# Performance work log

Hardware: AMD Instinct MI355X
Metric: run time of the kernel (lower is better)

## Reference

```python
import jax, jax.numpy as jnp
import numpy as np

T, S, B, E, H, F = 100, 4096, 32, 256, 8, 2048
DH = E // H
EPS = 1e-5

def setup_inputs() -> dict:
    key = jax.random.key(0)
    ks = jax.random.split(key, 32)
    n = lambda i, shape, s=1.0: jax.random.normal(ks[i], shape, jnp.float32) * s
    inp = {
        'hidden_states': n(0, (T, B, E)),
        'query_pos': n(1, (T, B, E)),
        'enc_hidden': n(2, (S, B, E)),
        'enc_pos': n(3, (S, B, E)),
        'attn_mask': n(4, (B * H, T, S)),
        # cross-attn (nn.MultiheadAttention) params
        'ca_wq': n(5, (E, E), 0.02), 'ca_bq': jnp.zeros(E),
        'ca_wk': n(6, (E, E), 0.02), 'ca_bk': jnp.zeros(E),
        'ca_wv': n(7, (E, E), 0.02), 'ca_bv': jnp.zeros(E),
        'ca_wo': n(8, (E, E), 0.02), 'ca_bo': jnp.zeros(E),
        # self-attn (Mask2FormerAttention) params
        'sa_wq': n(9, (E, E), 0.02), 'sa_bq': jnp.zeros(E),
        'sa_wk': n(10, (E, E), 0.02), 'sa_bk': jnp.zeros(E),
        'sa_wv': n(11, (E, E), 0.02), 'sa_bv': jnp.zeros(E),
        'sa_wo': n(12, (E, E), 0.02), 'sa_bo': jnp.zeros(E),
        # layer norms
        'ln1_g': jnp.ones(E), 'ln1_b': jnp.zeros(E),
        'ln2_g': jnp.ones(E), 'ln2_b': jnp.zeros(E),
        'ln3_g': jnp.ones(E), 'ln3_b': jnp.zeros(E),
        # FFN
        'fc1_w': n(13, (F, E), 0.02), 'fc1_b': jnp.zeros(F),
        'fc2_w': n(14, (E, F), 0.02), 'fc2_b': jnp.zeros(E),
    }
    return inp

def _ln(x, g, b):
    m = jnp.mean(x, -1, keepdims=True)
    v = jnp.mean(jnp.square(x - m), -1, keepdims=True)
    return (x - m) * jax.lax.rsqrt(v + EPS) * g + b

def _mha(q_in, k_in, v_in, wq, bq, wk, bk, wv, bv, wo, bo, mask):
    # q_in: [B,T,E], k_in/v_in: [B,S,E], mask: [B*H,T,S] additive or None
    b, t, _ = q_in.shape
    s = k_in.shape[1]
    q = (q_in @ wq.T + bq) * (DH ** -0.5)
    k = k_in @ wk.T + bk
    v = v_in @ wv.T + bv
    q = q.reshape(b, t, H, DH).transpose(0, 2, 1, 3)  # [B,H,T,dh]
    k = k.reshape(b, s, H, DH).transpose(0, 2, 1, 3)
    v = v.reshape(b, s, H, DH).transpose(0, 2, 1, 3)
    scores = jnp.einsum('bhtd,bhsd->bhts', q, k)
    if mask is not None:
        scores = scores + mask.reshape(b, H, t, s)
    p = jax.nn.softmax(scores, axis=-1)
    o = jnp.einsum('bhts,bhsd->bhtd', p, v)
    o = o.transpose(0, 2, 1, 3).reshape(b, t, E)
    return o @ wo.T + bo

def reference(hidden_states, query_pos, enc_hidden, enc_pos, attn_mask,
              ca_wq, ca_bq, ca_wk, ca_bk, ca_wv, ca_bv, ca_wo, ca_bo,
              sa_wq, sa_bq, sa_wk, sa_bk, sa_wv, sa_bv, sa_wo, sa_bo,
              ln1_g, ln1_b, ln2_g, ln2_b, ln3_g, ln3_b,
              fc1_w, fc1_b, fc2_w, fc2_b):
    # convert seq-first [T,B,E] -> batch-first [B,T,E]
    hs = hidden_states.transpose(1, 0, 2)
    qp = query_pos.transpose(1, 0, 2)
    enc = enc_hidden.transpose(1, 0, 2)
    ep = enc_pos.transpose(1, 0, 2)
    # masked cross-attention (post-norm), dropout=0
    residual = hs
    x = _mha(hs + qp, enc + ep, enc,
             ca_wq, ca_bq, ca_wk, ca_bk, ca_wv, ca_bv, ca_wo, ca_bo, attn_mask)
    hs = _ln(residual + x, ln1_g, ln1_b)
    # self-attention with query pos embeddings on q and k, no mask
    residual = hs
    x = _mha(hs + qp, hs + qp, hs,
             sa_wq, sa_bq, sa_wk, sa_bk, sa_wv, sa_bv, sa_wo, sa_bo, None)
    hs = _ln(residual + x, ln2_g, ln2_b)
    # FFN
    x = jax.nn.relu(hs @ fc1_w.T + fc1_b) @ fc2_w.T + fc2_b
    hs = _ln(hs + x, ln3_g, ln3_b)
    return hs.transpose(1, 0, 2)  # back to [T,B,E]
```

## Files before the change

### kernel.cpp

```cpp
#include <hip/hip_runtime.h>
#include <hip/hip_bf16.h>
#include <math.h>

#define TQ 100
#define SS 4096
#define BB 32
#define EE 256
#define HH 8
#define FF 2048
#define DHH 32
#define LNEPS 1e-5f

typedef __attribute__((ext_vector_type(8))) short bf16x8;
typedef __attribute__((ext_vector_type(4))) short bf16x4;
typedef __attribute__((ext_vector_type(4))) float f32x4;

__device__ inline unsigned short f2bfu(float f) {
    __hip_bfloat16 h = __float2bfloat16(f);
    return *reinterpret_cast<unsigned short*>(&h);
}

#define PBM 64
#define PBK 32
#define PLDP 40
#define TLP 268

__global__ __launch_bounds__(256)
void cvt_all(const float* s0, const float* s1, const float* s2, const float* s3,
             const float* s4, const float* s5, const float* s6, const float* s7,
             const float* s8, const float* s9,
             unsigned short* d0, unsigned short* d1, unsigned short* d2, unsigned short* d3,
             unsigned short* d4, unsigned short* d5, unsigned short* d6, unsigned short* d7,
             unsigned short* d8, unsigned short* d9)
{
    const int bi = blockIdx.x;
    const float* s; unsigned short* d; int base;
    if (bi < 512) {
        const int seg = bi >> 6;
        base = (bi & 63) * 1024;
        switch (seg) {
            case 0: s = s0; d = d0; break;
            case 1: s = s1; d = d1; break;
            case 2: s = s2; d = d2; break;
            case 3: s = s3; d = d3; break;
            case 4: s = s4; d = d4; break;
            case 5: s = s5; d = d5; break;
            case 6: s = s6; d = d6; break;
            default: s = s7; d = d7; break;
        }
    } else {
        const int r = bi - 512;
        base = (r & 511) * 1024;
        if (r >> 9) { s = s9; d = d9; } else { s = s8; d = d8; }
    }
    const int i = base + threadIdx.x * 4;
    float4 v = *(const float4*)(s + i);
    ushort4 ov;
    ov.x = f2bfu(v.x); ov.y = f2bfu(v.y); ov.z = f2bfu(v.z); ov.w = f2bfu(v.w);
    *(ushort4*)(d + i) = ov;
}

__global__ __launch_bounds__(512, 4)
void proj_kv(const float* __restrict__ enc, const float* __restrict__ ep,
             const __hip_bfloat16* __restrict__ Wk, const float* __restrict__ bk,
             const __hip_bfloat16* __restrict__ Wv, const float* __restrict__ bv,
             __hip_bfloat16* __restrict__ Kout, __hip_bfloat16* __restrict__ Vtout)
{
    __shared__ short Akv[PBM][PLDP];
    __shared__ short Av[PBM][PLDP];
    __shared__ short BkRaw[256 * PLDP];
    __shared__ short BvRaw[256 * PLDP];
    short (*Bk)[PLDP] = (short(*)[PLDP])BkRaw;
    short (*Bv)[PLDP] = (short(*)[PLDP])BvRaw;
    short (*tk)[TLP] = (short(*)[TLP])BkRaw;
    short (*tv)[TLP] = (short(*)[TLP])BvRaw;

    const int tid = threadIdx.x;
    const int m0 = blockIdx.x * PBM;
    const int b = m0 >> 12;
    const int s0 = m0 & (SS - 1);

    const int arr = tid >> 3;
    const int arc = (tid & 7) << 2;
    const long long abase = ((long long)(s0 + arr) * BB + b) * EE + arc;
    const int wr = tid >> 1;
    const int wc = (tid & 1) << 4;
    const long long wbase = (long long)wr * EE + wc;

    const int w = tid >> 6, l = tid & 63;
    const int mat = w >> 2;
    const int wm0 = (w & 1) * 32;
    const int wn0 = ((w >> 1) & 1) * 128;
    const int lr16 = l & 15, lk8 = (l >> 4) * 8;

    f32x4 acc[2][8] = {};

    float4 a0 = *(const float4*)(enc + abase);
    float4 e0 = *(const float4*)(ep + abase);

    for (int k0 = 0; k0 < EE; k0 += PBK) {
        bf16x8 wk8a = *(const bf16x8*)(Wk + wbase + k0);
        bf16x8 wk8b = *(const bf16x8*)(Wk + wbase + k0 + 8);
        bf16x8 wv8a = *(const bf16x8*)(Wv + wbase + k0);
        bf16x8 wv8b = *(const bf16x8*)(Wv + wbase + k0 + 8);

        bf16x4 pv, pkv;
        pv[0] = (short)f2bfu(a0.x); pv[1] = (short)f2bfu(a0.y);
        pv[2] = (short)f2bfu(a0.z); pv[3] = (short)f2bfu(a0.w);
        pkv[0] = (short)f2bfu(a0.x + e0.x); pkv[1] = (short)f2bfu(a0.y + e0.y);
        pkv[2] = (short)f2bfu(a0.z + e0.z); pkv[3] = (short)f2bfu(a0.w + e0.w);

        __syncthreads();
        *(bf16x4*)&Akv[arr][arc] = pkv;
        *(bf16x4*)&Av[arr][arc]  = pv;
        *(bf16x8*)&Bk[wr][wc]     = wk8a;
        *(bf16x8*)&Bk[wr][wc + 8] = wk8b;
        *(bf16x8*)&Bv[wr][wc]     = wv8a;
        *(bf16x8*)&Bv[wr][wc + 8] = wv8b;
        __syncthreads();

        if (k0 + PBK < EE) {
            a0 = *(const float4*)(enc + abase + k0 + PBK);
            e0 = *(const float4*)(ep + abase + k0 + PBK);
        }

        const short (*Am)[PLDP] = mat ? Av : Akv;
        const short (*Bm)[PLDP] = mat ? Bv : Bk;
        bf16x8 af0 = *(const bf16x8*)&Am[wm0 + lr16][lk8];
        bf16x8 af1 = *(const bf16x8*)&Am[wm0 + 16 + lr16][lk8];
        #pragma unroll
        for (int j = 0; j < 8; ++j) {
            bf16x8 b8 = *(const bf16x8*)&Bm[wn0 + j * 16 + lr16][lk8];
            acc[0][j] = __builtin_amdgcn_mfma_f32_16x16x32_bf16(af0, b8, acc[0][j], 0, 0, 0);
            acc[1][j] = __builtin_amdgcn_mfma_f32_16x16x32_bf16(af1, b8, acc[1][j], 0, 0, 0);
        }
    }

    const float* bias = mat ? bv : bk;
    const int q4 = (l >> 4) * 4;
    #pragma unroll
    for (int h = 0; h < 2; ++h) {
        __syncthreads();
        if (wm0 == h * 32) {
            short (*tile)[TLP] = mat ? tv : tk;
            #pragma unroll
            for (int i = 0; i < 2; ++i) {
                #pragma unroll
                for (int j = 0; j < 8; ++j) {
                    const int n = wn0 + j * 16 + lr16;
                    const float bi = bias[n];
                    #pragma unroll
                    for (int r = 0; r < 4; ++r)
                        tile[i * 16 + q4 + r][n] = (short)f2bfu(acc[i][j][r] + bi);
                }
            }
        }
        __syncthreads();
        #pragma unroll
        for (int it = 0; it < 4; ++it) {
            const int r2 = w * 4 + it;
            ushort4 v = *(const ushort4*)&tk[r2][l * 4];
            *(ushort4*)(Kout + (long long)(m0 + h * 32 + r2) * EE + l * 4) = v;
        }
        #pragma unroll
        for (int nn = 0; nn < 16; ++nn) {
            const int n = w * 32 + nn * 2 + (l >> 5);
            const int s = l & 31;
            unsigned short v = (unsigned short)tv[s][n];
            *((unsigned short*)Vtout + (long long)(b * EE + n) * SS + s0 + h * 32 + s) = v;
        }
    }
}

template<int A1G, int A2Q, int A1BF, int OBF, int RELU>
__global__ __launch_bounds__(128)
void mfma_gemm2(const void* __restrict__ A1v, const float* __restrict__ A2,
                const __hip_bfloat16* __restrict__ Wb, const float* __restrict__ bias,
                void* __restrict__ outv, int N, int K, float scale)
{
    __shared__ short As[32][PLDP];
    __shared__ short Bs[128][PLDP];
    const int tid = threadIdx.x;
    const int m0 = blockIdx.x * 32;
    const int n0 = blockIdx.y * 128;
    const int rr = tid >> 2;
    const int rc = (tid & 3) << 3;
    const int row = m0 + rr;

    long long a2row = 0;
    if (A1G || A2Q) {
        int bq = row / TQ, tq = row - bq * TQ;
        a2row = ((long long)(tq * BB + bq)) * EE;
    }
    const long long a1row = A1G ? a2row : (long long)row * K;

    const int wv = tid >> 6, l = tid & 63;
    const int wm0 = wv * 16;
    const int lr16 = l & 15, lk8 = (l >> 4) * 8;

    f32x4 acc[8] = {};

    for (int k0 = 0; k0 < K; k0 += PBK) {
        bf16x8 apack;
        if (A1BF) {
            apack = *(const bf16x8*)((const __hip_bfloat16*)A1v + a1row + k0 + rc);
        } else {
            const float* A1 = (const float*)A1v;
            float4 a0 = *(const float4*)(A1 + a1row + k0 + rc);
            float4 a1 = *(const float4*)(A1 + a1row + k0 + rc + 4);
            if (A2Q) {
                float4 e0 = *(const float4*)(A2 + a2row + k0 + rc);
                float4 e1 = *(const float4*)(A2 + a2row + k0 + rc + 4);
                a0.x += e0.x; a0.y += e0.y; a0.z += e0.z; a0.w += e0.w;
                a1.x += e1.x; a1.y += e1.y; a1.z += e1.z; a1.w += e1.w;
            }
            apack[0] = (short)f2bfu(a0.x); apack[1] = (short)f2bfu(a0.y);
            apack[2] = (short)f2bfu(a0.z); apack[3] = (short)f2bfu(a0.w);
            apack[4] = (short)f2bfu(a1.x); apack[5] = (short)f2bfu(a1.y);
            apack[6] = (short)f2bfu(a1.z); apack[7] = (short)f2bfu(a1.w);
        }

        bf16x8 wreg[4];
        #pragma unroll
        for (int it = 0; it < 4; ++it)
            wreg[it] = *(const bf16x8*)(Wb + (long long)(n0 + rr + it * 32) * K + k0 + rc);

        __syncthreads();
        *(bf16x8*)&As[rr][rc] = apack;
        #pragma unroll
        for (int it = 0; it < 4; ++it)
            *(bf16x8*)&Bs[rr + it * 32][rc] = wreg[it];
        __syncthreads();

        bf16x8 af = *(const bf16x8*)&As[wm0 + lr16][lk8];
        #pragma unroll
        for (int j = 0; j < 8; ++j) {
            bf16x8 bfr = *(const bf16x8*)&Bs[j * 16 + lr16][lk8];
            acc[j] = __builtin_amdgcn_mfma_f32_16x16x32_bf16(af, bfr, acc[j], 0, 0, 0);
        }
    }

    const int q4 = (l >> 4) * 4;
    #pragma unroll
    for (int j = 0; j < 8; ++j) {
        const int n = n0 + j * 16 + lr16;
        const float bi = bias[n];
        #pragma unroll
        for (int r = 0; r < 4; ++r) {
            float v = (acc[j][r] + bi) * scale;
            if (RELU) v = fmaxf(v, 0.f);
            const long long oidx = (long long)(m0 + wm0 + q4 + r) * N + n;
            if (OBF) ((__hip_bfloat16*)outv)[oidx] = __float2bfloat16(v);
            else     ((float*)outv)[oidx] = v;
        }
    }
}

__global__ __launch_bounds__(128)
void qkv_sa(const float* __restrict__ hs1, const float* __restrict__ qp,
            const __hip_bfloat16* __restrict__ Wq, const float* __restrict__ bq,
            const __hip_bfloat16* __restrict__ Wk, const float* __restrict__ bk,
            const __hip_bfloat16* __restrict__ Wv, const float* __restrict__ bv,
            __hip_bfloat16* __restrict__ Qs, __hip_bfloat16* __restrict__ Ks,
            __hip_bfloat16* __restrict__ Vt, int SVT, float qscale)
{
    __shared__ short Aq[32][PLDP];
    __shared__ short Av[32][PLDP];
    __shared__ short Bq[128][PLDP];
    __shared__ short Bk[128][PLDP];
    __shared__ short Bv[128][PLDP];
    const int tid = threadIdx.x;
    const int m0 = blockIdx.x * 32;
    const int n0 = blockIdx.y * 128;
    const int rr = tid >> 2;
    const int rc = (tid & 3) << 3;
    const int row = m0 + rr;
    const int bq_ = row / TQ, tq = row - bq_ * TQ;
    const long long a1row = (long long)row * EE;
    const long long a2row = ((long long)(tq * BB + bq_)) * EE;

    const int wv = tid >> 6, l = tid & 63;
    const int wm0 = wv * 16;
    const int lr16 = l & 15, lk8 = (l >> 4) * 8;

    f32x4 aq[8] = {}, ak[8] = {}, av[8] = {};

    for (int k0 = 0; k0 < EE; k0 += PBK) {
        float4 a0 = *(const float4*)(hs1 + a1row + k0 + rc);
        float4 a1 = *(const float4*)(hs1 + a1row + k0 + rc + 4);
        float4 e0 = *(const float4*)(qp + a2row + k0 + rc);
        float4 e1 = *(const float4*)(qp + a2row + k0 + rc + 4);
        bf16x8 pq, pv;
        pv[0] = (short)f2bfu(a0.x); pv[1] = (short)f2bfu(a0.y);
        pv[2] = (short)f2bfu(a0.z); pv[3] = (short)f2bfu(a0.w);
        pv[4] = (short)f2bfu(a1.x); pv[5] = (short)f2bfu(a1.y);
        pv[6] = (short)f2bfu(a1.z); pv[7] = (short)f2bfu(a1.w);
        pq[0] = (short)f2bfu(a0.x + e0.x); pq[1] = (short)f2bfu(a0.y + e0.y);
        pq[2] = (short)f2bfu(a0.z + e0.z); pq[3] = (short)f2bfu(a0.w + e0.w);
        pq[4] = (short)f2bfu(a1.x + e1.x); pq[5] = (short)f2bfu(a1.y + e1.y);
        pq[6] = (short)f2bfu(a1.z + e1.z); pq[7] = (short)f2bfu(a1.w + e1.w);

        bf16x8 wq8[4], wk8[4], wv8[4];
        #pragma unroll
        for (int it = 0; it < 4; ++it) {
            const long long wr = (long long)(n0 + rr + it * 32) * EE + k0 + rc;
            wq8[it] = *(const bf16x8*)(Wq + wr);
            wk8[it] = *(const bf16x8*)(Wk + wr);
            wv8[it] = *(const bf16x8*)(Wv + wr);
        }

        __syncthreads();
        *(bf16x8*)&Aq[rr][rc] = pq;
        *(bf16x8*)&Av[rr][rc] = pv;
        #pragma unroll
        for (int it = 0; it < 4; ++it) {
            *(bf16x8*)&Bq[rr + it * 32][rc] = wq8[it];
            *(bf16x8*)&Bk[rr + it * 32][rc] = wk8[it];
            *(bf16x8*)&Bv[rr + it * 32][rc] = wv8[it];
        }
        __syncthreads();

        bf16x8 afq = *(const bf16x8*)&Aq[wm0 + lr16][lk8];
        bf16x8 afv = *(const bf16x8*)&Av[wm0 + lr16][lk8];
        #pragma unroll
        for (int j = 0; j < 8; ++j) {
            bf16x8 b1 = *(const bf16x8*)&Bq[j * 16 + lr16][lk8];
            bf16x8 b2 = *(const bf16x8*)&Bk[j * 16 + lr16][lk8];
            bf16x8 b3 = *(const bf16x8*)&Bv[j * 16 + lr16][lk8];
            aq[j] = __builtin_amdgcn_mfma_f32_16x16x32_bf16(afq, b1, aq[j], 0, 0, 0);
            ak[j] = __builtin_amdgcn_mfma_f32_16x16x32_bf16(afq, b2, ak[j], 0, 0, 0);
            av[j] = __builtin_amdgcn_mfma_f32_16x16x32_bf16(afv, b3, av[j], 0, 0, 0);
        }
    }

    const int q4 = (l >> 4) * 4;
    #pragma unroll
    for (int j = 0; j < 8; ++j) {
        const int n = n0 + j * 16 + lr16;
        const float b1 = bq[n], b2 = bk[n], b3 = bv[n];
        #pragma unroll
        for (int r = 0; r < 4; ++r) {
            const int m = m0 + wm0 + q4 + r;
            Qs[(long long)m * EE + n] = __float2bfloat16((aq[j][r] + b1) * qscale);
            Ks[(long long)m * EE + n] = __float2bfloat16(ak[j][r] + b2);
            const int bb = m / TQ, tt = m - bb * TQ;
            Vt[(long long)(bb * EE + n) * SVT + tt] = __float2bfloat16(av[j][r] + b3);
        }
    }
}

#define KVB 32
#define LDP 40

__global__ __launch_bounds__(256, 2)
void flash_mfma(const __hip_bfloat16* __restrict__ Qg,
                const __hip_bfloat16* __restrict__ Kg,
                const __hip_bfloat16* __restrict__ Vtg,
                const float* __restrict__ mask,
                __hip_bfloat16* __restrict__ O,
                int Skv, int SVT)
{
    __shared__ short Ks[2][KVB][LDP];
    __shared__ short Vs[2][KVB][LDP];
    const int tid = threadIdx.x;
    const int l = tid & 63;
    const int g = l >> 4, q16 = l & 15;
    const int chunk = gridDim.x >> 3;
    const int logical = (blockIdx.x & 7) * chunk + (blockIdx.x >> 3);
    const int qb = logical & 1;
    const int bh = logical >> 1;
    const int h = bh & (HH - 1), b = bh >> 3;
    const int q0 = qb * 64 + (tid >> 6) * 16;

    int qc = q0 + q16; if (qc >= TQ) qc = TQ - 1;
    const bf16x8 qfrag = *(const bf16x8*)(Qg + ((long long)(b * TQ + qc)) * EE + h * DHH + g * 8);

    const int srow = tid >> 3;
    const int sseg = (tid & 7) * 4;
    const long long kbase = ((long long)b * Skv) * EE + h * DHH;
    const long long vbase = ((long long)(b * EE + h * DHH)) * SVT;
    const float* mrowp = mask ? mask + ((long long)bh * TQ + qc) * Skv : nullptr;

    f32x4 oacc[2] = {{0.f,0.f,0.f,0.f},{0.f,0.f,0.f,0.f}};
    float mrun = -1e30f, lrun = 0.f;
    const f32x4 zero = {0.f,0.f,0.f,0.f};

    int s_ld = srow; if (s_ld >= Skv) s_ld = Skv - 1;
    bf16x4 kreg = *(const bf16x4*)(Kg + kbase + (long long)s_ld * EE + sseg);
    bf16x4 vreg = *(const bf16x4*)(Vtg + vbase + (long long)srow * SVT + sseg);
    float4 mcur0, mcur1;
    if (mrowp) {
        mcur0 = *(const float4*)(mrowp + g * 4);
        mcur1 = *(const float4*)(mrowp + 16 + g * 4);
    }

    const int nround = (Skv + KVB - 1) / KVB;
    for (int r = 0; r < nround; ++r) {
        const int buf = r & 1;
        *(bf16x4*)&Ks[buf][srow][sseg] = kreg;
        *(bf16x4*)&Vs[buf][srow][sseg] = vreg;
        float4 mnx0, mnx1;
        if (r + 1 < nround) {
            int sn = (r + 1) * KVB + srow; if (sn >= Skv) sn = Skv - 1;
            kreg = *(const bf16x4*)(Kg + kbase + (long long)sn * EE + sseg);
            vreg = *(const bf16x4*)(Vtg + vbase + (long long)srow * SVT + (r + 1) * KVB + sseg);
            if (mrowp) {
                mnx0 = *(const float4*)(mrowp + (r + 1) * KVB + g * 4);
                mnx1 = *(const float4*)(mrowp + (r + 1) * KVB + 16 + g * 4);
            }
        }
        __syncthreads();

        const int s0 = r * KVB;
        f32x4 sT[2];
        #pragma unroll
        for (int t = 0; t < 2; ++t) {
            bf16x8 kf = *(const bf16x8*)&Ks[buf][t * 16 + q16][g * 8];
            sT[t] = __builtin_amdgcn_mfma_f32_16x16x32_bf16(kf, qfrag, zero, 0, 0, 0);
        }
        float sc[8];
        if (mrowp) {
            sc[0] = sT[0][0] + mcur0.x; sc[1] = sT[0][1] + mcur0.y;
            sc[2] = sT[0][2] + mcur0.z; sc[3] = sT[0][3] + mcur0.w;
            sc[4] = sT[1][0] + mcur1.x; sc[5] = sT[1][1] + mcur1.y;
            sc[6] = sT[1][2] + mcur1.z; sc[7] = sT[1][3] + mcur1.w;
        } else {
            #pragma unroll
            for (int t = 0; t < 2; ++t)
                #pragma unroll
                for (int rg = 0; rg < 4; ++rg) {
                    int s = s0 + t * 16 + g * 4 + rg;
                    sc[t*4+rg] = (s < Skv) ? sT[t][rg] : -1e30f;
                }
        }
        float tmax = sc[0];
        #pragma unroll
        for (int i = 1; i < 8; ++i) tmax = fmaxf(tmax, sc[i]);
        tmax = fmaxf(tmax, __shfl_xor(tmax, 16));
        tmax = fmaxf(tmax, __shfl_xor(tmax, 32));
        const float mn = fmaxf(mrun, tmax);
        const float corr = __expf(mrun - mn);
        mrun = mn;
        float ps = 0.f;
        bf16x8 pfrag;
        #pragma unroll
        for (int i = 0; i < 8; ++i) {
            float p = __expf(sc[i] - mn);
            ps += p;
            pfrag[i] = (short)f2bfu(p);
        }
        ps += __shfl_xor(ps, 16);
        ps += __shfl_xor(ps, 32);
        lrun = lrun * corr + ps;
        #pragma unroll
        for (int rg = 0; rg < 4; ++rg) {
            float c = __shfl(corr, g * 4 + rg);
            oacc[0][rg] *= c;
            oacc[1][rg] *= c;
        }
        #pragma unroll
        for (int T = 0; T < 2; ++T) {
            bf16x4 v0 = *(const bf16x4*)&Vs[buf][T * 16 + q16][g * 4];
            bf16x4 v1 = *(const bf16x4*)&Vs[buf][T * 16 + q16][16 + g * 4];
            bf16x8 vf;
            vf[0] = v0[0]; vf[1] = v0[1]; vf[2] = v0[2]; vf[3] = v0[3];
            vf[4] = v1[0]; vf[5] = v1[1]; vf[6] = v1[2]; vf[7] = v1[3];
            oacc[T] = __builtin_amdgcn_mfma_f32_16x16x32_bf16(pfrag, vf, oacc[T], 0, 0, 0);
        }
        mcur0 = mnx0; mcur1 = mnx1;
        __syncthreads();
    }

    float linv[4];
    #pragma unroll
    for (int rg = 0; rg < 4; ++rg)
        linv[rg] = 1.f / __shfl(lrun, g * 4 + rg);
    #pragma unroll
    for (int rg = 0; rg < 4; ++rg) {
        const int q = q0 + g * 4 + rg;
        if (q < TQ) {
            __hip_bfloat16* op = O + ((long long)(b * TQ + q)) * EE + h * DHH + q16;
            op[0]  = __float2bfloat16(oacc[0][rg] * linv[rg]);
            op[16] = __float2bfloat16(oacc[1][rg] * linv[rg]);
        }
    }
}

template<int GATHER_RES, int OUT_T, int OUT_BF>
__global__ __launch_bounds__(256)
void ln_kernel(const float* __restrict__ res, const float* __restrict__ x,
               const float* __restrict__ gam, const float* __restrict__ bet,
               float* __restrict__ out, __hip_bfloat16* __restrict__ outb)
{
    __shared__ float r1[4], r2[4];
    const int m = blockIdx.x;
    const int k = threadIdx.x;
    const int b = m / TQ, t = m - b * TQ;
    const long long roff = GATHER_RES ? ((long long)(t * BB + b)) * EE : (long long)m * EE;
    float v = res[roff + k] + x[(long long)m * EE + k];
    float s = v;
    #pragma unroll
    for (int off = 32; off; off >>= 1) s += __shfl_down(s, off);
    if ((k & 63) == 0) r1[k >> 6] = s;
    __syncthreads();
    const float mu = (r1[0] + r1[1] + r1[2] + r1[3]) * (1.0f / EE);
    const float d = v - mu;
    float s2 = d * d;
    #pragma unroll
    for (int off = 32; off; off >>= 1) s2 += __shfl_down(s2, off);
    if ((k & 63) == 0) r2[k >> 6] = s2;
    __syncthreads();
    const float var = (r2[0] + r2[1] + r2[2] + r2[3]) * (1.0f / EE);
    const float o = d * rsqrtf(var + LNEPS) * gam[k] + bet[k];
    const long long ooff = OUT_T ? ((long long)(t * BB + b)) * EE : (long long)m * EE;
    out[ooff + k] = o;
    if (OUT_BF) outb[(long long)m * EE + k] = __float2bfloat16(o);
}

extern "C" void kernel_launch(void* const* d_in, const int* in_sizes, int n_in,
                              void* d_out, int out_size, void* d_ws, size_t ws_size,
                              hipStream_t stream)
{
    const float* hs    = (const float*)d_in[0];
    const float* qp    = (const float*)d_in[1];
    const float* enc   = (const float*)d_in[2];
    const float* ep    = (const float*)d_in[3];
    const float* mask  = (const float*)d_in[4];
    const float* ca_wq = (const float*)d_in[5];  const float* ca_bq = (const float*)d_in[6];
    const float* ca_wk = (const float*)d_in[7];  const float* ca_bk = (const float*)d_in[8];
    const float* ca_wv = (const float*)d_in[9];  const float* ca_bv = (const float*)d_in[10];
    const float* ca_wo = (const float*)d_in[11]; const float* ca_bo = (const float*)d_in[12];
    const float* sa_wq = (const float*)d_in[13]; const float* sa_bq = (const float*)d_in[14];
    const float* sa_wk = (const float*)d_in[15]; const float* sa_bk = (const float*)d_in[16];
    const float* sa_wv = (const float*)d_in[17]; const float* sa_bv = (const float*)d_in[18];
    const float* sa_wo = (const float*)d_in[19]; const float* sa_bo = (const float*)d_in[20];
    const float* ln1_g = (const float*)d_in[21]; const float* ln1_b = (const float*)d_in[22];
    const float* ln2_g = (const float*)d_in[23]; const float* ln2_b = (const float*)d_in[24];
    const float* ln3_g = (const float*)d_in[25]; const float* ln3_b = (const float*)d_in[26];
    const float* fc1_w = (const float*)d_in[27]; const float* fc1_b = (const float*)d_in[28];
    const float* fc2_w = (const float*)d_in[29]; const float* fc2_b = (const float*)d_in[30];

    const int MQ = BB * TQ;
    const int MK = BB * SS;
    const int SVT2 = 128;

    size_t off = 0;
    char* base = (char*)d_ws;
    auto alloc = [&](size_t bytes) -> void* {
        void* p = base + off; off = (off + bytes + 255) & ~(size_t)255; return p;
    };
    __hip_bfloat16* Kc  = (__hip_bfloat16*)alloc((size_t)MK * EE * 2);
    __hip_bfloat16* Vt  = (__hip_bfloat16*)alloc((size_t)BB * EE * SS * 2);
    __hip_bfloat16* Qc  = (__hip_bfloat16*)alloc((size_t)MQ * EE * 2);
    __hip_bfloat16* Qs  = (__hip_bfloat16*)alloc((size_t)MQ * EE * 2);
    __hip_bfloat16* Ks2 = (__hip_bfloat16*)alloc((size_t)MQ * EE * 2);
    __hip_bfloat16* Vt2 = (__hip_bfloat16*)alloc((size_t)BB * EE * SVT2 * 2);
    __hip_bfloat16* Wq1 = (__hip_bfloat16*)alloc((size_t)EE * EE * 2);
    __hip_bfloat16* Wkb = (__hip_bfloat16*)alloc((size_t)EE * EE * 2);
    __hip_bfloat16* Wvb = (__hip_bfloat16*)alloc((size_t)EE * EE * 2);
    __hip_bfloat16* Wo1 = (__hip_bfloat16*)alloc((size_t)EE * EE * 2);
    __hip_bfloat16* Wq2 = (__hip_bfloat16*)alloc((size_t)EE * EE * 2);
    __hip_bfloat16* Wk2 = (__hip_bfloat16*)alloc((size_t)EE * EE * 2);
    __hip_bfloat16* Wv2 = (__hip_bfloat16*)alloc((size_t)EE * EE * 2);
    __hip_bfloat16* Wo2 = (__hip_bfloat16*)alloc((size_t)EE * EE * 2);
    __hip_bfloat16* Wf1 = (__hip_bfloat16*)alloc((size_t)FF * EE * 2);
    __hip_bfloat16* Wf2 = (__hip_bfloat16*)alloc((size_t)EE * FF * 2);
    __hip_bfloat16* hs2b= (__hip_bfloat16*)alloc((size_t)MQ * EE * 2);
    __hip_bfloat16* h1b = (__hip_bfloat16*)alloc((size_t)MQ * FF * 2);
    __hip_bfloat16* attO  = (__hip_bfloat16*)alloc((size_t)MQ * EE * 2);
    __hip_bfloat16* attO2 = (__hip_bfloat16*)alloc((size_t)MQ * EE * 2);
    float* xproj = (float*)alloc((size_t)MQ * EE * 4);
    float* hs1   = (float*)alloc((size_t)MQ * EE * 4);
    float* xpro2 = (float*)alloc((size_t)MQ * EE * 4);
    float* hs2   = (float*)alloc((size_t)MQ * EE * 4);
    float* xffn  = (float*)alloc((size_t)MQ * EE * 4);

    const float qscale = 0.17677669529663687f;
    dim3 blk(256);

    cvt_all<<<dim3(1536), blk, 0, stream>>>(
        ca_wq, ca_wk, ca_wv, ca_wo, sa_wq, sa_wk, sa_wv, sa_wo, fc1_w, fc2_w,
        (unsigned short*)Wq1, (unsigned short*)Wkb, (unsigned short*)Wvb,
        (unsigned short*)Wo1, (unsigned short*)Wq2, (unsigned short*)Wk2,
        (unsigned short*)Wv2, (unsigned short*)Wo2, (unsigned short*)Wf1,
        (unsigned short*)Wf2);

    mfma_gemm2<1,1,0,1,0><<<dim3(MQ/32, 2), dim3(128), 0, stream>>>(hs, qp, Wq1, ca_bq, Qc, EE, EE, qscale);
    proj_kv<<<dim3(MK/PBM), dim3(512), 0, stream>>>(enc, ep, Wkb, ca_bk, Wvb, ca_bv, Kc, Vt);
    flash_mfma<<<dim3(BB*HH*2), dim3(256), 0, stream>>>(Qc, Kc, Vt, mask, attO, SS, SS);
    mfma_gemm2<0,0,1,0,0><<<dim3(MQ/32, 2), dim3(128), 0, stream>>>(attO, nullptr, Wo1, ca_bo, xproj, EE, EE, 1.f);
    ln_kernel<1,0,0><<<dim3(MQ), blk, 0, stream>>>(hs, xproj, ln1_g, ln1_b, hs1, nullptr);

    qkv_sa<<<dim3(MQ/32, 2), dim3(128), 0, stream>>>(hs1, qp, Wq2, sa_bq, Wk2, sa_bk, Wv2, sa_bv,
                                                     Qs, Ks2, Vt2, SVT2, qscale);
    flash_mfma<<<dim3(BB*HH*2), dim3(256), 0, stream>>>(Qs, Ks2, Vt2, nullptr, attO2, TQ, SVT2);
    mfma_gemm2<0,0,1,0,0><<<dim3(MQ/32, 2), dim3(128), 0, stream>>>(attO2, nullptr, Wo2, sa_bo, xpro2, EE, EE, 1.f);
    ln_kernel<0,0,1><<<dim3(MQ), blk, 0, stream>>>(hs1, xpro2, ln2_g, ln2_b, hs2, hs2b);

    mfma_gemm2<0,0,1,1,1><<<dim3(MQ/32, FF/128), dim3(128), 0, stream>>>(hs2b, nullptr, Wf1, fc1_b, h1b, FF, EE, 1.f);
    mfma_gemm2<0,0,1,0,0><<<dim3(MQ/32, 2), dim3(128), 0, stream>>>(h1b, nullptr, Wf2, fc2_b, xffn, EE, FF, 1.f);
    ln_kernel<0,1,0><<<dim3(MQ), blk, 0, stream>>>(hs2, xffn, ln3_g, ln3_b, (float*)d_out, nullptr);

    (void)in_sizes; (void)n_in; (void)out_size; (void)ws_size;
}
```

Measured before the change: 378.1 us.

## Restructure proj_kv: smaller tiles, weights from global, double-buffered A tile

The K/V projection kernel now uses 32-row tiles with 256 threads instead of 64 rows with 512. Weight fragments are read straight from global memory (L2/L1) into registers rather than staged through LDS. The activation tile is double-buffered in LDS so there is one barrier per K step instead of two. This shrinks LDS use to allow higher occupancy and removes the weight staging traffic, but it repeats weight loads from global per wave and makes each block do more serialized epilogue passes for K and V through a single shared tile.

```diff
diff --git a/kernel.cpp b/kernel.cpp
--- a/kernel.cpp
+++ b/kernel.cpp
@@ -60,115 +60,130 @@
     *(ushort4*)(d + i) = ov;
 }
 
-__global__ __launch_bounds__(512, 4)
+__global__ __launch_bounds__(256, 4)
 void proj_kv(const float* __restrict__ enc, const float* __restrict__ ep,
              const __hip_bfloat16* __restrict__ Wk, const float* __restrict__ bk,
              const __hip_bfloat16* __restrict__ Wv, const float* __restrict__ bv,
              __hip_bfloat16* __restrict__ Kout, __hip_bfloat16* __restrict__ Vtout)
 {
-    __shared__ short Akv[PBM][PLDP];
-    __shared__ short Av[PBM][PLDP];
-    __shared__ short BkRaw[256 * PLDP];
-    __shared__ short BvRaw[256 * PLDP];
-    short (*Bk)[PLDP] = (short(*)[PLDP])BkRaw;
-    short (*Bv)[PLDP] = (short(*)[PLDP])BvRaw;
-    short (*tk)[TLP] = (short(*)[TLP])BkRaw;
-    short (*tv)[TLP] = (short(*)[TLP])BvRaw;
-
+    __shared__ short lds[32 * TLP];
     const int tid = threadIdx.x;
-    const int m0 = blockIdx.x * PBM;
+    const int m0 = blockIdx.x * 32;
     const int b = m0 >> 12;
     const int s0 = m0 & (SS - 1);
 
     const int arr = tid >> 3;
     const int arc = (tid & 7) << 2;
     const long long abase = ((long long)(s0 + arr) * BB + b) * EE + arc;
-    const int wr = tid >> 1;
-    const int wc = (tid & 1) << 4;
-    const long long wbase = (long long)wr * EE + wc;
 
     const int w = tid >> 6, l = tid & 63;
-    const int mat = w >> 2;
-    const int wm0 = (w & 1) * 32;
-    const int wn0 = ((w >> 1) & 1) * 128;
+    const int mat = w >> 1;
+    const int wn0 = (w & 1) * 128;
     const int lr16 = l & 15, lk8 = (l >> 4) * 8;
+    const __hip_bfloat16* Wm = mat ? Wv : Wk;
+    const long long wlbase = (long long)(wn0 + lr16) * EE + lk8;
 
     f32x4 acc[2][8] = {};
 
     float4 a0 = *(const float4*)(enc + abase);
     float4 e0 = *(const float4*)(ep + abase);
-
-    for (int k0 = 0; k0 < EE; k0 += PBK) {
-        bf16x8 wk8a = *(const bf16x8*)(Wk + wbase + k0);
-        bf16x8 wk8b = *(const bf16x8*)(Wk + wbase + k0 + 8);
-        bf16x8 wv8a = *(const bf16x8*)(Wv + wbase + k0);
-        bf16x8 wv8b = *(const bf16x8*)(Wv + wbase + k0 + 8);
-
-        bf16x4 pv, pkv;
+    {
+        bf16x4 pk, pv;
+        pk[0] = (short)f2bfu(a0.x + e0.x); pk[1] = (short)f2bfu(a0.y + e0.y);
+        pk[2] = (short)f2bfu(a0.z + e0.z); pk[3] = (short)f2bfu(a0.w + e0.w);
         pv[0] = (short)f2bfu(a0.x); pv[1] = (short)f2bfu(a0.y);
         pv[2] = (short)f2bfu(a0.z); pv[3] = (short)f2bfu(a0.w);
-        pkv[0] = (short)f2bfu(a0.x + e0.x); pkv[1] = (short)f2bfu(a0.y + e0.y);
-        pkv[2] = (short)f2bfu(a0.z + e0.z); pkv[3] = (short)f2bfu(a0.w + e0.w);
-
+        *(bf16x4*)&lds[arr * PLDP + arc] = pk;
+        *(bf16x4*)&lds[2560 + arr * PLDP + arc] = pv;
+    }
+    __syncthreads();
+
+    int p = 0;
+    for (int k0 = 0; k0 < EE; k0 += PBK) {
+        float4 a1, e1;
+        const bool more = (k0 + PBK < EE);
+        if (more) {
+            a1 = *(const float4*)(enc + abase + k0 + PBK);
+            e1 = *(const float4*)(ep + abase + k0 + PBK);
+        }
+
+        const int ab = (mat ? 2560 : 0) + p * 1280;
+        bf16x8 af0 = *(const bf16x8*)&lds[ab + lr16 * PLDP + lk8];
+        bf16x8 af1 = *(const bf16x8*)&lds[ab + (16 + lr16) * PLDP + lk8];
+
+        bf16x8 wr[4];
+        #pragma unroll
+        for (int j = 0; j < 4; ++j)
+            wr[j] = *(const bf16x8*)(Wm + wlbase + (long long)(j * 16) * EE + k0);
+        #pragma unroll
+        for (int j = 0; j < 4; ++j) {
+            acc[0][j] = __builtin_amdgcn_mfma_f32_16x16x32_bf16(af0, wr[j], acc[0][j], 0, 0, 0);
+            acc[1][j] = __builtin_amdgcn_mfma_f32_16x16x32_bf16(af1, wr[j], acc[1][j], 0, 0, 0);
+        }
+        #pragma unroll
+        for (int j = 0; j < 4; ++j)
+            wr[j] = *(const bf16x8*)(Wm + wlbase + (long long)((j + 4) * 16) * EE + k0);
+        #pragma unroll
+        for (int j = 0; j < 4; ++j) {
+            acc[0][j + 4] = __builtin_amdgcn_mfma_f32_16x16x32_bf16(af0, wr[j], acc[0][j + 4], 0, 0, 0);
+            acc[1][j + 4] = __builtin_amdgcn_mfma_f32_16x16x32_bf16(af1, wr[j], acc[1][j + 4], 0, 0, 0);
+        }
+
+        if (more) {
+            bf16x4 pk, pv;
+            pk[0] = (short)f2bfu(a1.x + e1.x); pk[1] = (short)f2bfu(a1.y + e1.y);
+            pk[2] = (short)f2bfu(a1.z + e1.z); pk[3] = (short)f2bfu(a1.w + e1.w);
+            pv[0] = (short)f2bfu(a1.x); pv[1] = (short)f2bfu(a1.y);
+            pv[2] = (short)f2bfu(a1.z); pv[3] = (short)f2bfu(a1.w);
+            *(bf16x4*)&lds[(p ^ 1) * 1280 + arr * PLDP + arc] = pk;
+            *(bf16x4*)&lds[2560 + (p ^ 1) * 1280 + arr * PLDP + arc] = pv;
+        }
         __syncthreads();
-        *(bf16x4*)&Akv[arr][arc] = pkv;
-        *(bf16x4*)&Av[arr][arc]  = pv;
-        *(bf16x8*)&Bk[wr][wc]     = wk8a;
-        *(bf16x8*)&Bk[wr][wc + 8] = wk8b;
-        *(bf16x8*)&Bv[wr][wc]     = wv8a;
-        *(bf16x8*)&Bv[wr][wc + 8] = wv8b;
-        __syncthreads();
-
-        if (k0 + PBK < EE) {
-            a0 = *(const float4*)(enc + abase + k0 + PBK);
-            e0 = *(const float4*)(ep + abase + k0 + PBK);
-        }
-
-        const short (*Am)[PLDP] = mat ? Av : Akv;
-        const short (*Bm)[PLDP] = mat ? Bv : Bk;
-        bf16x8 af0 = *(const bf16x8*)&Am[wm0 + lr16][lk8];
-        bf16x8 af1 = *(const bf16x8*)&Am[wm0 + 16 + lr16][lk8];
-        #pragma unroll
-        for (int j = 0; j < 8; ++j) {
-            bf16x8 b8 = *(const bf16x8*)&Bm[wn0 + j * 16 + lr16][lk8];
-            acc[0][j] = __builtin_amdgcn_mfma_f32_16x16x32_bf16(af0, b8, acc[0][j], 0, 0, 0);
-            acc[1][j] = __builtin_amdgcn_mfma_f32_16x16x32_bf16(af1, b8, acc[1][j], 0, 0, 0);
-        }
-    }
-
-    const float* bias = mat ? bv : bk;
+        p ^= 1;
+    }
+
+    short (*tile)[TLP] = (short(*)[TLP])lds;
     const int q4 = (l >> 4) * 4;
-    #pragma unroll
-    for (int h = 0; h < 2; ++h) {
-        __syncthreads();
-        if (wm0 == h * 32) {
-            short (*tile)[TLP] = mat ? tv : tk;
+
+    if (mat == 0) {
+        #pragma unroll
+        for (int i = 0; i < 2; ++i)
             #pragma unroll
-            for (int i = 0; i < 2; ++i) {
+            for (int j = 0; j < 8; ++j) {
+                const int n = wn0 + j * 16 + lr16;
+                const float bi = bk[n];
                 #pragma unroll
-                for (int j = 0; j < 8; ++j) {
-                    const int n = wn0 + j * 16 + lr16;
-                    const float bi = bias[n];
-                    #pragma unroll
-                    for (int r = 0; r < 4; ++r)
-                        tile[i * 16 + q4 + r][n] = (short)f2bfu(acc[i][j][r] + bi);
-                }
+                for (int r = 0; r < 4; ++r)
+                    tile[i * 16 + q4 + r][n] = (short)f2bfu(acc[i][j][r] + bi);
             }
-        }
-        __syncthreads();
-        #pragma unroll
-        for (int it = 0; it < 4; ++it) {
-            const int r2 = w * 4 + it;
-            ushort4 v = *(const ushort4*)&tk[r2][l * 4];
-            *(ushort4*)(Kout + (long long)(m0 + h * 32 + r2) * EE + l * 4) = v;
-        }
-        #pragma unroll
-        for (int nn = 0; nn < 16; ++nn) {
-            const int n = w * 32 + nn * 2 + (l >> 5);
-            const int s = l & 31;
-            unsigned short v = (unsigned short)tv[s][n];
-            *((unsigned short*)Vtout + (long long)(b * EE + n) * SS + s0 + h * 32 + s) = v;
-        }
+    }
+    __syncthreads();
+    #pragma unroll
+    for (int it = 0; it < 8; ++it) {
+        const int r2 = w * 8 + it;
+        ushort4 v = *(const ushort4*)&tile[r2][l * 4];
+        *(ushort4*)(Kout + (long long)(m0 + r2) * EE + l * 4) = v;
+    }
+    __syncthreads();
+    if (mat == 1) {
+        #pragma unroll
+        for (int i = 0; i < 2; ++i)
+            #pragma unroll
+            for (int j = 0; j < 8; ++j) {
+                const int n = wn0 + j * 16 + lr16;
+                const float bi = bv[n];
+                #pragma unroll
+                for (int r = 0; r < 4; ++r)
+                    tile[i * 16 + q4 + r][n] = (short)f2bfu(acc[i][j][r] + bi);
+            }
+    }
+    __syncthreads();
+    #pragma unroll
+    for (int nn = 0; nn < 32; ++nn) {
+        const int n = w * 64 + nn * 2 + (l >> 5);
+        const int s = l & 31;
+        unsigned short v = (unsigned short)tile[s][n];
+        *((unsigned short*)Vtout + (long long)(b * EE + n) * SS + s0 + s) = v;
     }
 }
 
@@ -586,7 +601,7 @@
         (unsigned short*)Wf2);
 
     mfma_gemm2<1,1,0,1,0><<<dim3(MQ/32, 2), dim3(128), 0, stream>>>(hs, qp, Wq1, ca_bq, Qc, EE, EE, qscale);
-    proj_kv<<<dim3(MK/PBM), dim3(512), 0, stream>>>(enc, ep, Wkb, ca_bk, Wvb, ca_bv, Kc, Vt);
+    proj_kv<<<dim3(MK/32), blk, 0, stream>>>(enc, ep, Wkb, ca_bk, Wvb, ca_bv, Kc, Vt);
     flash_mfma<<<dim3(BB*HH*2), dim3(256), 0, stream>>>(Qc, Kc, Vt, mask, attO, SS, SS);
     mfma_gemm2<0,0,1,0,0><<<dim3(MQ/32, 2), dim3(128), 0, stream>>>(attO, nullptr, Wo1, ca_bo, xproj, EE, EE, 1.f);
     ln_kernel<1,0,0><<<dim3(MQ), blk, 0, stream>>>(hs, xproj, ln1_g, ln1_b, hs1, nullptr);
```

After: 433.2 us. +14.6%, slower.

## Widen flash attention KV tile to 64 and use one 512-thread block per head

Applied to the files above, without the earlier changes.

The flash attention kernel now processes 64 keys per round instead of 32 and runs one 512-thread block per (batch, head), covering all 100 queries with 8 waves. Previously two 256-thread blocks each reloaded the same K/V tiles. The aim is to halve K/V global traffic and halve the number of barrier rounds. In exchange the grid shrinks to 256 blocks, per-thread register pressure rises (16 scores plus 4 mask vectors), and the XCD-aware block remapping is dropped.

```diff
diff --git a/kernel.cpp b/kernel.cpp
--- a/kernel.cpp
+++ b/kernel.cpp
@@ -303,10 +303,10 @@
         bf16x8 wq8[4], wk8[4], wv8[4];
         #pragma unroll
         for (int it = 0; it < 4; ++it) {
-            const long long wr = (long long)(n0 + rr + it * 32) * EE + k0 + rc;
-            wq8[it] = *(const bf16x8*)(Wq + wr);
-            wk8[it] = *(const bf16x8*)(Wk + wr);
-            wv8[it] = *(const bf16x8*)(Wv + wr);
+            const long long wrx = (long long)(n0 + rr + it * 32) * EE + k0 + rc;
+            wq8[it] = *(const bf16x8*)(Wq + wrx);
+            wk8[it] = *(const bf16x8*)(Wk + wrx);
+            wv8[it] = *(const bf16x8*)(Wv + wrx);
         }
 
         __syncthreads();
@@ -349,10 +349,9 @@
     }
 }
 
-#define KVB 32
-#define LDP 40
-
-__global__ __launch_bounds__(256, 2)
+#define KVB 64
+
+__global__ __launch_bounds__(512, 2)
 void flash_mfma(const __hip_bfloat16* __restrict__ Qg,
                 const __hip_bfloat16* __restrict__ Kg,
                 const __hip_bfloat16* __restrict__ Vtg,
@@ -360,23 +359,22 @@
                 __hip_bfloat16* __restrict__ O,
                 int Skv, int SVT)
 {
-    __shared__ short Ks[2][KVB][LDP];
-    __shared__ short Vs[2][KVB][LDP];
+    __shared__ short Ks[2][KVB][40];
+    __shared__ short Vs[2][DHH][72];
     const int tid = threadIdx.x;
     const int l = tid & 63;
     const int g = l >> 4, q16 = l & 15;
-    const int chunk = gridDim.x >> 3;
-    const int logical = (blockIdx.x & 7) * chunk + (blockIdx.x >> 3);
-    const int qb = logical & 1;
-    const int bh = logical >> 1;
+    const int bh = blockIdx.x;
     const int h = bh & (HH - 1), b = bh >> 3;
-    const int q0 = qb * 64 + (tid >> 6) * 16;
+    const int q0 = (tid >> 6) * 16;
 
     int qc = q0 + q16; if (qc >= TQ) qc = TQ - 1;
     const bf16x8 qfrag = *(const bf16x8*)(Qg + ((long long)(b * TQ + qc)) * EE + h * DHH + g * 8);
 
-    const int srow = tid >> 3;
-    const int sseg = (tid & 7) * 4;
+    const int ksr = tid >> 3;
+    const int ksc = (tid & 7) * 4;
+    const int vsr = tid >> 4;
+    const int vsc = (tid & 15) * 4;
     const long long kbase = ((long long)b * Skv) * EE + h * DHH;
     const long long vbase = ((long long)(b * EE + h * DHH)) * SVT;
     const float* mrowp = mask ? mask + ((long long)bh * TQ + qc) * Skv : nullptr;
@@ -385,48 +383,49 @@
     float mrun = -1e30f, lrun = 0.f;
     const f32x4 zero = {0.f,0.f,0.f,0.f};
 
-    int s_ld = srow; if (s_ld >= Skv) s_ld = Skv - 1;
-    bf16x4 kreg = *(const bf16x4*)(Kg + kbase + (long long)s_ld * EE + sseg);
-    bf16x4 vreg = *(const bf16x4*)(Vtg + vbase + (long long)srow * SVT + sseg);
-    float4 mcur0, mcur1;
+    int s_ld = ksr; if (s_ld >= Skv) s_ld = Skv - 1;
+    bf16x4 kreg = *(const bf16x4*)(Kg + kbase + (long long)s_ld * EE + ksc);
+    bf16x4 vreg = *(const bf16x4*)(Vtg + vbase + (long long)vsr * SVT + vsc);
+    float4 mcur[4], mnx[4];
     if (mrowp) {
-        mcur0 = *(const float4*)(mrowp + g * 4);
-        mcur1 = *(const float4*)(mrowp + 16 + g * 4);
+        #pragma unroll
+        for (int t = 0; t < 4; ++t) mcur[t] = *(const float4*)(mrowp + t * 16 + g * 4);
     }
 
     const int nround = (Skv + KVB - 1) / KVB;
     for (int r = 0; r < nround; ++r) {
         const int buf = r & 1;
-        *(bf16x4*)&Ks[buf][srow][sseg] = kreg;
-        *(bf16x4*)&Vs[buf][srow][sseg] = vreg;
-        float4 mnx0, mnx1;
+        *(bf16x4*)&Ks[buf][ksr][ksc] = kreg;
+        *(bf16x4*)&Vs[buf][vsr][vsc] = vreg;
         if (r + 1 < nround) {
-            int sn = (r + 1) * KVB + srow; if (sn >= Skv) sn = Skv - 1;
-            kreg = *(const bf16x4*)(Kg + kbase + (long long)sn * EE + sseg);
-            vreg = *(const bf16x4*)(Vtg + vbase + (long long)srow * SVT + (r + 1) * KVB + sseg);
+            int sn = (r + 1) * KVB + ksr; if (sn >= Skv) sn = Skv - 1;
+            kreg = *(const bf16x4*)(Kg + kbase + (long long)sn * EE + ksc);
+            vreg = *(const bf16x4*)(Vtg + vbase + (long long)vsr * SVT + (r + 1) * KVB + vsc);
             if (mrowp) {
-                mnx0 = *(const float4*)(mrowp + (r + 1) * KVB + g * 4);
-                mnx1 = *(const float4*)(mrowp + (r + 1) * KVB + 16 + g * 4);
+                #pragma unroll
+                for (int t = 0; t < 4; ++t)
+                    mnx[t] = *(const float4*)(mrowp + (r + 1) * KVB + t * 16 + g * 4);
             }
         }
         __syncthreads();
 
         const int s0 = r * KVB;
-        f32x4 sT[2];
-        #pragma unroll
-        for (int t = 0; t < 2; ++t) {
+        f32x4 sT[4];
+        #pragma unroll
+        for (int t = 0; t < 4; ++t) {
             bf16x8 kf = *(const bf16x8*)&Ks[buf][t * 16 + q16][g * 8];
             sT[t] = __builtin_amdgcn_mfma_f32_16x16x32_bf16(kf, qfrag, zero, 0, 0, 0);
         }
-        float sc[8];
+        float sc[16];
         if (mrowp) {
-            sc[0] = sT[0][0] + mcur0.x; sc[1] = sT[0][1] + mcur0.y;
-            sc[2] = sT[0][2] + mcur0.z; sc[3] = sT[0][3] + mcur0.w;
-            sc[4] = sT[1][0] + mcur1.x; sc[5] = sT[1][1] + mcur1.y;
-            sc[6] = sT[1][2] + mcur1.z; sc[7] = sT[1][3] + mcur1.w;
+            #pragma unroll
+            for (int t = 0; t < 4; ++t) {
+                sc[t*4+0] = sT[t][0] + mcur[t].x; sc[t*4+1] = sT[t][1] + mcur[t].y;
+                sc[t*4+2] = sT[t][2] + mcur[t].z; sc[t*4+3] = sT[t][3] + mcur[t].w;
+            }
         } else {
             #pragma unroll
-            for (int t = 0; t < 2; ++t)
+            for (int t = 0; t < 4; ++t)
                 #pragma unroll
                 for (int rg = 0; rg < 4; ++rg) {
                     int s = s0 + t * 16 + g * 4 + rg;
@@ -435,19 +434,18 @@
         }
         float tmax = sc[0];
         #pragma unroll
-        for (int i = 1; i < 8; ++i) tmax = fmaxf(tmax, sc[i]);
+        for (int i = 1; i < 16; ++i) tmax = fmaxf(tmax, sc[i]);
         tmax = fmaxf(tmax, __shfl_xor(tmax, 16));
         tmax = fmaxf(tmax, __shfl_xor(tmax, 32));
         const float mn = fmaxf(mrun, tmax);
         const float corr = __expf(mrun - mn);
         mrun = mn;
         float ps = 0.f;
-        bf16x8 pfrag;
-        #pragma unroll
-        for (int i = 0; i < 8; ++i) {
-            float p = __expf(sc[i] - mn);
-            ps += p;
-            pfrag[i] = (short)f2bfu(p);
+        float pe[16];
+        #pragma unroll
+        for (int i = 0; i < 16; ++i) {
+            pe[i] = __expf(sc[i] - mn);
+            ps += pe[i];
         }
         ps += __shfl_xor(ps, 16);
         ps += __shfl_xor(ps, 32);
@@ -459,15 +457,25 @@
             oacc[1][rg] *= c;
         }
         #pragma unroll
-        for (int T = 0; T < 2; ++T) {
-            bf16x4 v0 = *(const bf16x4*)&Vs[buf][T * 16 + q16][g * 4];
-            bf16x4 v1 = *(const bf16x4*)&Vs[buf][T * 16 + q16][16 + g * 4];
-            bf16x8 vf;
-            vf[0] = v0[0]; vf[1] = v0[1]; vf[2] = v0[2]; vf[3] = v0[3];
-            vf[4] = v1[0]; vf[5] = v1[1]; vf[6] = v1[2]; vf[7] = v1[3];
-            oacc[T] = __builtin_amdgcn_mfma_f32_16x16x32_bf16(pfrag, vf, oacc[T], 0, 0, 0);
-        }
-        mcur0 = mnx0; mcur1 = mnx1;
+        for (int sb = 0; sb < 2; ++sb) {
+            bf16x8 pfrag;
+            #pragma unroll
+            for (int e = 0; e < 4; ++e) {
+                pfrag[e]     = (short)f2bfu(pe[(2*sb)*4 + e]);
+                pfrag[e + 4] = (short)f2bfu(pe[(2*sb+1)*4 + e]);
+            }
+            #pragma unroll
+            for (int T = 0; T < 2; ++T) {
+                bf16x4 v0 = *(const bf16x4*)&Vs[buf][T * 16 + q16][sb * 32 + g * 4];
+                bf16x4 v1 = *(const bf16x4*)&Vs[buf][T * 16 + q16][sb * 32 + 16 + g * 4];
+                bf16x8 vf;
+                vf[0] = v0[0]; vf[1] = v0[1]; vf[2] = v0[2]; vf[3] = v0[3];
+                vf[4] = v1[0]; vf[5] = v1[1]; vf[6] = v1[2]; vf[7] = v1[3];
+                oacc[T] = __builtin_amdgcn_mfma_f32_16x16x32_bf16(pfrag, vf, oacc[T], 0, 0, 0);
+            }
+        }
+        #pragma unroll
+        for (int t = 0; t < 4; ++t) mcur[t] = mnx[t];
         __syncthreads();
     }
 
@@ -587,13 +595,13 @@
 
     mfma_gemm2<1,1,0,1,0><<<dim3(MQ/32, 2), dim3(128), 0, stream>>>(hs, qp, Wq1, ca_bq, Qc, EE, EE, qscale);
     proj_kv<<<dim3(MK/PBM), dim3(512), 0, stream>>>(enc, ep, Wkb, ca_bk, Wvb, ca_bv, Kc, Vt);
-    flash_mfma<<<dim3(BB*HH*2), dim3(256), 0, stream>>>(Qc, Kc, Vt, mask, attO, SS, SS);
+    flash_mfma<<<dim3(BB*HH), dim3(512), 0, stream>>>(Qc, Kc, Vt, mask, attO, SS, SS);
     mfma_gemm2<0,0,1,0,0><<<dim3(MQ/32, 2), dim3(128), 0, stream>>>(attO, nullptr, Wo1, ca_bo, xproj, EE, EE, 1.f);
     ln_kernel<1,0,0><<<dim3(MQ), blk, 0, stream>>>(hs, xproj, ln1_g, ln1_b, hs1, nullptr);
 
     qkv_sa<<<dim3(MQ/32, 2), dim3(128), 0, stream>>>(hs1, qp, Wq2, sa_bq, Wk2, sa_bk, Wv2, sa_bv,
                                                      Qs, Ks2, Vt2, SVT2, qscale);
-    flash_mfma<<<dim3(BB*HH*2), dim3(256), 0, stream>>>(Qs, Ks2, Vt2, nullptr, attO2, TQ, SVT2);
+    flash_mfma<<<dim3(BB*HH), dim3(512), 0, stream>>>(Qs, Ks2, Vt2, nullptr, attO2, TQ, SVT2);
     mfma_gemm2<0,0,1,0,0><<<dim3(MQ/32, 2), dim3(128), 0, stream>>>(attO2, nullptr, Wo2, sa_bo, xpro2, EE, EE, 1.f);
     ln_kernel<0,0,1><<<dim3(MQ), blk, 0, stream>>>(hs1, xpro2, ln2_g, ln2_b, hs2, hs2b);
 
```

Result: faster. 366.7 us (-3.0%).
